# Performance work log

Measured on AMD Instinct MI355X. Metric: run time of the kernel, lower is better.

Reference implementation:

```python
import jax, jax.numpy as jnp
import numpy as np

B, L, D, H, FF = 2, 2048, 1024, 16, 4096


def _xavier(key, out_d, in_d):
    lim = (6.0 / (in_d + out_d)) ** 0.5
    return jax.random.uniform(key, (out_d, in_d), jnp.float32, -lim, lim)


def setup_inputs() -> dict:
    key = jax.random.key(0)
    ks = jax.random.split(key, 7)
    x = jax.random.normal(ks[0], (B, L, D), dtype=jnp.float32)
    wq = _xavier(ks[1], D, D)
    wk = _xavier(ks[2], D, D)
    wv = _xavier(ks[3], D, D)
    wo = _xavier(ks[4], D, D)
    w1 = _xavier(ks[5], FF, D)
    w2 = _xavier(ks[6], D, FF)
    zD = jnp.zeros((D,), jnp.float32)
    return dict(x=x, wq=wq, bq=zD, wk=wk, bk=zD, wv=wv, bv=zD, wo=wo, bo=zD,
                w1=w1, b1=jnp.zeros((FF,), jnp.float32), w2=w2, b2=zD)


def _ln2d(x, eps=1e-5):
    # F.layer_norm(x, x.shape[1:]): normalize jointly over (L, D), no affine
    mu = jnp.mean(x, axis=(1, 2), keepdims=True)
    var = jnp.var(x, axis=(1, 2), keepdims=True)
    return (x - mu) * jax.lax.rsqrt(var + eps)


def reference(x, wq, bq, wk, bk, wv, bv, wo, bo, w1, b1, w2, b2):
    Bx, Lx, Dx = x.shape
    nH = H
    Dh = Dx // nH
    h = _ln2d(x)
    q = (h @ wq.T + bq).reshape(Bx, Lx, nH, Dh).transpose(0, 2, 1, 3)  # (B,H,L,Dh)
    k = (h @ wk.T + bk).reshape(Bx, Lx, nH, Dh).transpose(0, 2, 1, 3)
    v = (h @ wv.T + bv).reshape(Bx, Lx, nH, Dh).transpose(0, 2, 1, 3)
    # NOTE: faithful to source bug: scale = 1/sqrt(key.size(dim=1)) = 1/sqrt(num_heads)
    scale = 1.0 / jnp.sqrt(jnp.asarray(nH, jnp.float32))
    att = jax.nn.softmax(jnp.einsum('bhqd,bhkd->bhqk', q, k) * scale, axis=-1)
    o = jnp.einsum('bhqk,bhkd->bhqd', att, v).transpose(0, 2, 1, 3).reshape(Bx, Lx, Dx)
    o = o @ wo.T + bo
    y = _ln2d(o + x)
    ff = jax.nn.relu(y @ w1.T + b1) @ w2.T + b2
    return ff + x  # second residual adds the ORIGINAL x (as in source)
```

## Files before the change

kernel.cpp:

```cpp
#include <hip/hip_runtime.h>
#include <cstdint>
#include <cstddef>

typedef unsigned short u16;
typedef unsigned int uint;
typedef __bf16 bf16x8 __attribute__((ext_vector_type(8)));
typedef float f32x4 __attribute__((ext_vector_type(4)));

#define BATCH 2
#define SEQ 2048
#define DIM 1024
#define NH 16
#define DH 64
#define FFD 4096
#define MROWS 4096
#define PER_BATCH 2097152

__device__ __forceinline__ u16 f2b(float f) {
  uint u = __builtin_bit_cast(uint, f);
  u += 0x7FFFu + ((u >> 16) & 1u);
  return (u16)(u >> 16);
}

__device__ __forceinline__ uint pkbf2(float a, float b) {
  u16 x = __builtin_bit_cast(u16, (__bf16)a);
  u16 y = __builtin_bit_cast(u16, (__bf16)b);
  return (uint)x | ((uint)y << 16);
}

__device__ __forceinline__ int xcd_swz(int flat, int nwg) {
  return (flat & 7) * (nwg >> 3) + (flat >> 3);
}

#define GLL(gp, lp)                                                            \
  __builtin_amdgcn_global_load_lds(                                            \
      (const __attribute__((address_space(1))) void*)(gp),                     \
      (__attribute__((address_space(3))) void*)(lp), 16, 0, 0)

__global__ __launch_bounds__(256) void cvt4_kernel(const float* __restrict__ s0,
                                                   const float* __restrict__ s1,
                                                   const float* __restrict__ s2,
                                                   const float* __restrict__ s3,
                                                   u16* d0, u16* d1, u16* d2, u16* d3,
                                                   int n) {
  int t = blockIdx.y;
  const float* src = (t == 0) ? s0 : (t == 1) ? s1 : (t == 2) ? s2 : s3;
  u16* dst = (t == 0) ? d0 : (t == 1) ? d1 : (t == 2) ? d2 : d3;
  int i = (blockIdx.x * 256 + threadIdx.x) * 8;
  if (i >= n) return;
  float4 a = *(const float4*)(src + i);
  float4 b = *(const float4*)(src + i + 4);
  uint4 o;
  o.x = f2b(a.x) | ((uint)f2b(a.y) << 16);
  o.y = f2b(a.z) | ((uint)f2b(a.w) << 16);
  o.z = f2b(b.x) | ((uint)f2b(b.y) << 16);
  o.w = f2b(b.z) | ((uint)f2b(b.w) << 16);
  *(uint4*)(dst + i) = o;
}

__global__ __launch_bounds__(256) void reduce_stats_kernel(const float* __restrict__ x,
                                                           float* __restrict__ stats) {
  int b = blockIdx.y;
  const float* p = x + (size_t)b * PER_BATCH;
  float s = 0.f, ss = 0.f;
  int stride = gridDim.x * 256 * 4;
  for (int i = (blockIdx.x * 256 + threadIdx.x) * 4; i < PER_BATCH; i += stride) {
    float4 v = *(const float4*)(p + i);
    s  += (v.x + v.y) + (v.z + v.w);
    ss += (v.x * v.x + v.y * v.y) + (v.z * v.z + v.w * v.w);
  }
#pragma unroll
  for (int m = 32; m; m >>= 1) { s += __shfl_xor(s, m); ss += __shfl_xor(ss, m); }
  __shared__ float red[16];
  int w = threadIdx.x >> 6;
  if ((threadIdx.x & 63) == 0) { red[w] = s; red[8 + w] = ss; }
  __syncthreads();
  if (threadIdx.x == 0) {
    atomicAdd(&stats[b * 2],     red[0] + red[1] + red[2] + red[3]);
    atomicAdd(&stats[b * 2 + 1], red[8] + red[9] + red[10] + red[11]);
  }
}

__global__ __launch_bounds__(256) void ln_apply_kernel(const float* __restrict__ xin,
                                                       const float* __restrict__ stats,
                                                       u16* __restrict__ out) {
  int i = (blockIdx.x * 256 + threadIdx.x) * 4;
  int b = i >> 21;
  const float inv = 1.f / (float)PER_BATCH;
  float mu = stats[b * 2] * inv;
  float var = stats[b * 2 + 1] * inv - mu * mu;
  float rs = rsqrtf(var + 1e-5f);
  float4 v = *(const float4*)(xin + i);
  uint r0 = f2b((v.x - mu) * rs) | ((uint)f2b((v.y - mu) * rs) << 16);
  uint r1 = f2b((v.z - mu) * rs) | ((uint)f2b((v.w - mu) * rs) << 16);
  *(uint2*)(out + i) = make_uint2(r0, r1);
}

template <int TN, int RELU, int RESID, int OUTBF, int DBUF>
__device__ __forceinline__ void gemm_bt_body(const u16* __restrict__ A,
                                             const u16* __restrict__ Bm,
                                             const float* __restrict__ bias,
                                             const float* __restrict__ resid,
                                             void* __restrict__ Cout,
                                             int M, int N, int K,
                                             int m0, int n0, float oscale, int trv) {
  constexpr int AI  = (TN == 128) ? 4 : 2;
  constexpr int BCH = (TN == 128) ? 4 : 2;
  constexpr int NB  = DBUF ? 3 : 1;
  __shared__ __align__(16) u16 As[NB][128 * 64];
  __shared__ __align__(16) u16 Bs[NB][TN * 64];
  const int tid = threadIdx.x;
  const int lane = tid & 63, w = tid >> 6;
  const int wr = (TN == 128) ? (w >> 1) : w;
  const int wc = (TN == 128) ? (w & 1) : 0;
  const int ln = lane & 15, qd = lane >> 4;

  f32x4 acc[AI][4] = {};

  const int lrow = lane >> 3;
  const int scl  = (lane & 7) ^ lrow;
  const u16* Ag = A  + (size_t)(m0 + w * 32 + lrow) * K + scl * 8;
  const u16* Bg = Bm + (size_t)(n0 + w * 8 * BCH + lrow) * K + scl * 8;

  const int co0 = ((qd)     ^ (ln & 7)) * 8;
  const int co1 = ((4 + qd) ^ (ln & 7)) * 8;

  auto STAGE = [&](int buf, int k0) {
#pragma unroll
    for (int r = 0; r < 4; ++r)
      GLL(Ag + (size_t)(r * 8) * K + k0, As[buf] + (w * 4 + r) * 512);
#pragma unroll
    for (int r = 0; r < BCH; ++r)
      GLL(Bg + (size_t)(r * 8) * K + k0, Bs[buf] + (w * BCH + r) * 512);
  };

  auto COMPUTE = [&](int buf) {
#pragma unroll
    for (int kk = 0; kk < 2; ++kk) {
      const int co = kk ? co1 : co0;
      bf16x8 af[AI], bf[4];
#pragma unroll
      for (int t = 0; t < AI; ++t)
        af[t] = *(const bf16x8*)&As[buf][(wr * (AI * 16) + t * 16 + ln) * 64 + co];
#pragma unroll
      for (int t = 0; t < 4; ++t)
        bf[t] = *(const bf16x8*)&Bs[buf][(wc * 64 + t * 16 + ln) * 64 + co];
#pragma unroll
      for (int i = 0; i < AI; ++i)
#pragma unroll
        for (int j = 0; j < 4; ++j)
          acc[i][j] = __builtin_amdgcn_mfma_f32_16x16x32_bf16(af[i], bf[j], acc[i][j], 0, 0, 0);
    }
  };

  if constexpr (NB == 3) {
    const int nk = K >> 6;
    STAGE(0, 0);
    STAGE(1, 64);
    int c = 0, s = 2;
    int t = 0;
    for (; t + 1 < nk; ++t) {
      asm volatile("s_waitcnt vmcnt(6)" ::: "memory");
      __builtin_amdgcn_s_barrier();
      __builtin_amdgcn_sched_barrier(0);
      if (t + 2 < nk) STAGE(s, (t + 2) * 64);
      COMPUTE(c);
      c = (c == 2) ? 0 : c + 1;
      s = (s == 2) ? 0 : s + 1;
    }
    asm volatile("s_waitcnt vmcnt(0)" ::: "memory");
    __builtin_amdgcn_s_barrier();
    __builtin_amdgcn_sched_barrier(0);
    COMPUTE(c);
  } else {
    for (int k0 = 0; k0 < K; k0 += 64) {
      __syncthreads();
      STAGE(0, k0);
      __syncthreads();
      COMPUTE(0);
    }
  }

#pragma unroll
  for (int i = 0; i < AI; ++i) {
    int row = m0 + wr * (AI * 16) + i * 16 + qd * 4;
#pragma unroll
    for (int j = 0; j < 4; ++j) {
      int col = n0 + wc * 64 + j * 16 + ln;
      float bv = bias[col];
      if (trv) {
        union { uint2 u2; u16 us[4]; } pk;
#pragma unroll
        for (int r = 0; r < 4; ++r) pk.us[r] = f2b(acc[i][j][r] + bv);
        *(uint2*)&((u16*)Cout)[(size_t)col * MROWS + row] = pk.u2;
      } else {
#pragma unroll
        for (int r = 0; r < 4; ++r) {
          float v = (acc[i][j][r] + bv) * oscale;
          if (RELU) v = fmaxf(v, 0.f);
          size_t off = (size_t)(row + r) * N + col;
          if (RESID) v += resid[off];
          if (OUTBF) ((u16*)Cout)[off] = f2b(v);
          else       ((float*)Cout)[off] = v;
        }
      }
    }
  }
}

template <int TN, int RELU, int RESID, int OUTBF, int DBUF>
__global__ __launch_bounds__(256) void gemm_bt_kernel(const u16* __restrict__ A,
                                                      const u16* __restrict__ Bm,
                                                      const float* __restrict__ bias,
                                                      const float* __restrict__ resid,
                                                      void* __restrict__ Cout,
                                                      int M, int N, int K) {
  const int nx = gridDim.x;
  const int nwg = nx * gridDim.y;
  const int wid = xcd_swz(blockIdx.x + nx * blockIdx.y, nwg);
  gemm_bt_body<TN, RELU, RESID, OUTBF, DBUF>(A, Bm, bias, resid, Cout,
                                             M, N, K,
                                             (wid / nx) * 128, (wid % nx) * TN,
                                             1.0f, 0);
}

__global__ __launch_bounds__(256) void gemm_qkv_kernel(const u16* __restrict__ A,
                                                       const u16* B0, const u16* B1, const u16* B2,
                                                       const float* c0, const float* c1, const float* c2,
                                                       u16* o0, u16* o1, u16* o2) {
  int z = blockIdx.z;
  const int wid = xcd_swz(blockIdx.x + 16 * blockIdx.y, 512);
  const int m0 = (wid >> 4) * 128, n0 = (wid & 15) * 64;
  const u16* Bm = (z == 0) ? B0 : (z == 1) ? B1 : B2;
  const float* bias = (z == 0) ? c0 : (z == 1) ? c1 : c2;
  u16* Cout = (z == 0) ? o0 : (z == 1) ? o1 : o2;
  const float sc = (z == 0) ? 0.25f : 1.0f;
  gemm_bt_body<64, 0, 0, 1, 1>(A, Bm, bias, nullptr, Cout,
                               MROWS, DIM, DIM, m0, n0, sc, z == 2);
}

template <int RELU>
__global__ __launch_bounds__(512, 2) void gemm256_kernel(const u16* __restrict__ A,
                                                         const u16* __restrict__ Bm,
                                                         const float* __restrict__ bias,
                                                         u16* __restrict__ Cout,
                                                         int M, int N, int K) {
  __shared__ __align__(16) u16 As[2][256 * 64];
  __shared__ __align__(16) u16 Bs[2][256 * 64];
  const int tid = threadIdx.x;
  const int lane = tid & 63, w = tid >> 6;
  const int wr = w >> 2, wc = w & 3;
  const int ln = lane & 15, qd = lane >> 4;

  const int nx = gridDim.x;
  const int nwg = nx * gridDim.y;
  const int wid = xcd_swz(blockIdx.x + nx * blockIdx.y, nwg);
  const int m0 = (wid / nx) * 256, n0 = (wid % nx) * 256;

  f32x4 acc[8][4] = {};

  const int lrow = lane >> 3;
  const int scl  = (lane & 7) ^ lrow;
  const u16* Ag = A  + (size_t)(m0 + w * 32 + lrow) * K + scl * 8;
  const u16* Bg = Bm + (size_t)(n0 + w * 32 + lrow) * K + scl * 8;

  const int co0 = ((qd)     ^ (ln & 7)) * 8;
  const int co1 = ((4 + qd) ^ (ln & 7)) * 8;

  auto STAGE = [&](int buf, int k0) {
#pragma unroll
    for (int r = 0; r < 4; ++r) {
      GLL(Ag + (size_t)(r * 8) * K + k0, As[buf] + (w * 4 + r) * 512);
      GLL(Bg + (size_t)(r * 8) * K + k0, Bs[buf] + (w * 4 + r) * 512);
    }
  };

  auto COMPUTE = [&](int buf) {
#pragma unroll
    for (int kk = 0; kk < 2; ++kk) {
      const int co = kk ? co1 : co0;
      bf16x8 af[8], bf[4];
#pragma unroll
      for (int t = 0; t < 8; ++t)
        af[t] = *(const bf16x8*)&As[buf][(wr * 128 + t * 16 + ln) * 64 + co];
#pragma unroll
      for (int t = 0; t < 4; ++t)
        bf[t] = *(const bf16x8*)&Bs[buf][(wc * 64 + t * 16 + ln) * 64 + co];
      __builtin_amdgcn_s_setprio(1);
#pragma unroll
      for (int i = 0; i < 8; ++i)
#pragma unroll
        for (int j = 0; j < 4; ++j)
          acc[i][j] = __builtin_amdgcn_mfma_f32_16x16x32_bf16(af[i], bf[j], acc[i][j], 0, 0, 0);
      __builtin_amdgcn_s_setprio(0);
    }
  };

  const int nk = K >> 6;
  STAGE(0, 0);
  for (int t = 0; t < nk; ++t) {
    const int p = t & 1;
    __syncthreads();
    if (t + 1 < nk) STAGE(1 - p, (t + 1) * 64);
    COMPUTE(p);
  }

#pragma unroll
  for (int i = 0; i < 8; ++i) {
    int row = m0 + wr * 128 + i * 16 + qd * 4;
#pragma unroll
    for (int j = 0; j < 4; ++j) {
      int col = n0 + wc * 64 + j * 16 + ln;
      float bv = bias[col];
#pragma unroll
      for (int r = 0; r < 4; ++r) {
        float v = acc[i][j][r] + bv;
        if (RELU) v = fmaxf(v, 0.f);
        Cout[(size_t)(row + r) * N + col] = f2b(v);
      }
    }
  }
}

__global__ __launch_bounds__(256, 2) void attn_kernel(const u16* __restrict__ Q,
                                                      const u16* __restrict__ Km,
                                                      const u16* __restrict__ vT,
                                                      u16* __restrict__ O) {
  __shared__ __align__(16) u16 Ks[2][64 * 64];
  __shared__ __align__(16) u16 Vt[2][64 * 64];
  __shared__ __align__(16) u16 Ps[4][32 * 64];

  const int tid = threadIdx.x, lane = tid & 63, w = tid >> 6;
  const int ln = lane & 15, qd = lane >> 4;
  const int flat = blockIdx.x + 16 * (blockIdx.y + 16 * blockIdx.z);
  const int wid = xcd_swz(flat, 512);
  const int qi = wid & 15, head = (wid >> 4) & 15, b = wid >> 8;
  const int wq0 = b * SEQ + qi * 128 + w * 32;
  const int hcol = head * DH;

  bf16x8 qf[2][2];
#pragma unroll
  for (int ti = 0; ti < 2; ++ti)
#pragma unroll
    for (int kk = 0; kk < 2; ++kk)
      qf[ti][kk] = *(const bf16x8*)&Q[(size_t)(wq0 + ti * 16 + ln) * DIM + hcol + kk * 32 + qd * 8];

  union { u16 u[8]; bf16x8 v; } oneu;
#pragma unroll
  for (int e = 0; e < 8; ++e) oneu.u[e] = 0x3F80;
  const bf16x8 vones = oneu.v;

  f32x4 accO[2][4] = {};
  f32x4 accL[2] = {};

  const int srow = lane >> 3;
  const int scl  = (lane & 7) ^ srow;
  const u16* Kg = Km + (size_t)(b * SEQ + w * 16 + srow) * DIM + hcol + scl * 8;
  const u16* Vg = vT + (size_t)(hcol + w * 16 + srow) * MROWS + b * SEQ + scl * 8;
  u16* Pw = Ps[w];
  const int swz = ln & 7;

#pragma unroll
  for (int r = 0; r < 2; ++r) {
    GLL(Kg + (size_t)(r * 8) * DIM,   &Ks[0][(w * 2 + r) * 512]);
    GLL(Vg + (size_t)(r * 8) * MROWS, &Vt[0][(w * 2 + r) * 512]);
  }

  for (int t = 0; t < SEQ / 64; ++t) {
    const int p = t & 1;
    const int kt = t * 64;
    __syncthreads();

    if (t + 1 < SEQ / 64) {
      const int kt2 = kt + 64;
#pragma unroll
      for (int r = 0; r < 2; ++r) {
        GLL(Kg + (size_t)(kt2 + r * 8) * DIM,   &Ks[1 - p][(w * 2 + r) * 512]);
        GLL(Vg + (size_t)(r * 8) * MROWS + kt2, &Vt[1 - p][(w * 2 + r) * 512]);
      }
    }

    f32x4 sacc[4][2] = {};
#pragma unroll
    for (int kk = 0; kk < 2; ++kk) {
      bf16x8 kf[4];
#pragma unroll
      for (int tj = 0; tj < 4; ++tj)
        kf[tj] = *(const bf16x8*)&Ks[p][(tj * 16 + ln) * 64 + (((kk * 4 + qd) ^ swz) * 8)];
      __builtin_amdgcn_s_setprio(1);
#pragma unroll
      for (int tj = 0; tj < 4; ++tj)
#pragma unroll
        for (int ti = 0; ti < 2; ++ti)
          sacc[tj][ti] = __builtin_amdgcn_mfma_f32_16x16x32_bf16(kf[tj], qf[ti][kk], sacc[tj][ti], 0, 0, 0);
      __builtin_amdgcn_s_setprio(0);
    }

#pragma unroll
    for (int tj = 0; tj < 4; ++tj)
#pragma unroll
      for (int ti = 0; ti < 2; ++ti) {
        uint lo = pkbf2(__expf(sacc[tj][ti][0]), __expf(sacc[tj][ti][1]));
        uint hi = pkbf2(__expf(sacc[tj][ti][2]), __expf(sacc[tj][ti][3]));
        *(uint2*)&Pw[(ti * 16 + ln) * 64 + (((2 * tj + (qd >> 1)) ^ swz) * 8) + (qd & 1) * 4] =
            make_uint2(lo, hi);
      }

#pragma unroll
    for (int kk = 0; kk < 2; ++kk) {
      bf16x8 pf[2], vf[4];
#pragma unroll
      for (int ti = 0; ti < 2; ++ti)
        pf[ti] = *(const bf16x8*)&Pw[(ti * 16 + ln) * 64 + (((kk * 4 + qd) ^ swz) * 8)];
#pragma unroll
      for (int tjv = 0; tjv < 4; ++tjv)
        vf[tjv] = *(const bf16x8*)&Vt[p][(tjv * 16 + ln) * 64 + (((kk * 4 + qd) ^ swz) * 8)];
      __builtin_amdgcn_s_setprio(1);
#pragma unroll
      for (int ti = 0; ti < 2; ++ti) {
#pragma unroll
        for (int tjv = 0; tjv < 4; ++tjv)
          accO[ti][tjv] = __builtin_amdgcn_mfma_f32_16x16x32_bf16(pf[ti], vf[tjv], accO[ti][tjv], 0, 0, 0);
        accL[ti] = __builtin_amdgcn_mfma_f32_16x16x32_bf16(pf[ti], vones, accL[ti], 0, 0, 0);
      }
      __builtin_amdgcn_s_setprio(0);
    }
  }

#pragma unroll
  for (int ti = 0; ti < 2; ++ti)
#pragma unroll
    for (int r = 0; r < 4; ++r) {
      float inv = 1.f / accL[ti][r];
#pragma unroll
      for (int tjv = 0; tjv < 4; ++tjv)
        O[(size_t)(wq0 + ti * 16 + qd * 4 + r) * DIM + hcol + tjv * 16 + ln] =
            f2b(accO[ti][tjv][r] * inv);
    }
}

extern "C" void kernel_launch(void* const* d_in, const int* in_sizes, int n_in,
                              void* d_out, int out_size, void* d_ws, size_t ws_size,
                              hipStream_t stream) {
  const float* x  = (const float*)d_in[0];
  const float* wq = (const float*)d_in[1];
  const float* bq = (const float*)d_in[2];
  const float* wk = (const float*)d_in[3];
  const float* bk = (const float*)d_in[4];
  const float* wv = (const float*)d_in[5];
  const float* bv = (const float*)d_in[6];
  const float* wo = (const float*)d_in[7];
  const float* bo = (const float*)d_in[8];
  const float* w1 = (const float*)d_in[9];
  const float* b1 = (const float*)d_in[10];
  const float* w2 = (const float*)d_in[11];
  const float* b2 = (const float*)d_in[12];
  float* out = (float*)d_out;
  char* ws = (char*)d_ws;

  const size_t MB = 1u << 20;
  u16*   h    = (u16*)(ws + 0);
  u16*   q    = (u16*)(ws + 8  * MB);
  u16*   k    = (u16*)(ws + 16 * MB);
  u16*   v    = (u16*)(ws + 24 * MB);
  u16*   o    = (u16*)(ws + 32 * MB);
  u16*   r    = (u16*)(ws + 8  * MB);
  float* ares = (float*)(ws + 40 * MB);
  u16*   wqb  = (u16*)(ws + 56 * MB);
  u16*   wkb  = (u16*)(ws + 58 * MB);
  u16*   wvb  = (u16*)(ws + 60 * MB);
  u16*   wob  = (u16*)(ws + 62 * MB);
  u16*   w1b  = (u16*)(ws + 64 * MB);
  u16*   w2b  = (u16*)(ws + 72 * MB);
  float* stats= (float*)(ws + 80 * MB);
  u16*   y    = h;

  (void)hipMemsetAsync(stats, 0, 64, stream);

  cvt4_kernel<<<dim3(512, 4),  256, 0, stream>>>(wq, wk, wv, wo, wqb, wkb, wvb, wob, DIM * DIM);
  cvt4_kernel<<<dim3(2048, 2), 256, 0, stream>>>(w1, w2, w1, w2, w1b, w2b, w1b, w2b, FFD * DIM);

  reduce_stats_kernel<<<dim3(64, 2), 256, 0, stream>>>(x, stats);
  ln_apply_kernel<<<4096, 256, 0, stream>>>(x, stats, h);

  gemm_qkv_kernel<<<dim3(16, 32, 3), 256, 0, stream>>>(h, wqb, wkb, wvb, bq, bk, bv, q, k, v);

  attn_kernel<<<dim3(16, 16, 2), 256, 0, stream>>>(q, k, v, o);

  gemm_bt_kernel<64, 0, 1, 0, 1><<<dim3(16, 32), 256, 0, stream>>>(o, wob, bo, x, ares, MROWS, DIM, DIM);

  reduce_stats_kernel<<<dim3(64, 2), 256, 0, stream>>>(ares, stats + 4);
  ln_apply_kernel<<<4096, 256, 0, stream>>>(ares, stats + 4, y);

  gemm256_kernel<1><<<dim3(16, 16), 512, 0, stream>>>(y, w1b, b1, r, MROWS, FFD, DIM);

  gemm_bt_kernel<64, 0, 1, 0, 1><<<dim3(16, 32), 256, 0, stream>>>(r, w2b, b2, x, out, MROWS, DIM, FFD);
}
```

Before: 357.1 us.

## Fuse QKV projections into one GEMM sharing A tiles; merge weight conversions

Replaces the z-dimension QKV launch (three separate GEMMs that each reload the same activation tile) with one kernel. Each workgroup loads its 128x64 A tile once and multiplies it against the matching tiles of all three weight matrices, with a double-buffered LDS pipeline. The two weight-conversion launches are also merged into one six-way launch. This cuts redundant A traffic and a launch, at the cost of triple the accumulator registers (96 floats per lane), larger LDS use, lower occupancy, and only 512 workgroups instead of 1536.

```diff
diff --git a/kernel.cpp b/kernel.cpp
--- a/kernel.cpp
+++ b/kernel.cpp
@@ -37,15 +37,20 @@
       (const __attribute__((address_space(1))) void*)(gp),                     \
       (__attribute__((address_space(3))) void*)(lp), 16, 0, 0)
 
-__global__ __launch_bounds__(256) void cvt4_kernel(const float* __restrict__ s0,
+__global__ __launch_bounds__(256) void cvt6_kernel(const float* __restrict__ s0,
                                                    const float* __restrict__ s1,
                                                    const float* __restrict__ s2,
                                                    const float* __restrict__ s3,
-                                                   u16* d0, u16* d1, u16* d2, u16* d3,
-                                                   int n) {
+                                                   const float* __restrict__ s4,
+                                                   const float* __restrict__ s5,
+                                                   u16* d0, u16* d1, u16* d2,
+                                                   u16* d3, u16* d4, u16* d5) {
   int t = blockIdx.y;
-  const float* src = (t == 0) ? s0 : (t == 1) ? s1 : (t == 2) ? s2 : s3;
-  u16* dst = (t == 0) ? d0 : (t == 1) ? d1 : (t == 2) ? d2 : d3;
+  const float* src = (t == 0) ? s0 : (t == 1) ? s1 : (t == 2) ? s2
+                   : (t == 3) ? s3 : (t == 4) ? s4 : s5;
+  u16* dst = (t == 0) ? d0 : (t == 1) ? d1 : (t == 2) ? d2
+           : (t == 3) ? d3 : (t == 4) ? d4 : d5;
+  int n = (t < 4) ? DIM * DIM : FFD * DIM;
   int i = (blockIdx.x * 256 + threadIdx.x) * 8;
   if (i >= n) return;
   float4 a = *(const float4*)(src + i);
@@ -224,19 +229,104 @@
                                              1.0f, 0);
 }
 
-__global__ __launch_bounds__(256) void gemm_qkv_kernel(const u16* __restrict__ A,
-                                                       const u16* B0, const u16* B1, const u16* B2,
-                                                       const float* c0, const float* c1, const float* c2,
-                                                       u16* o0, u16* o1, u16* o2) {
-  int z = blockIdx.z;
+__global__ __launch_bounds__(256) void gemm_qkv3_kernel(const u16* __restrict__ A,
+                                                        const u16* __restrict__ B0,
+                                                        const u16* __restrict__ B1,
+                                                        const u16* __restrict__ B2,
+                                                        const float* __restrict__ c0,
+                                                        const float* __restrict__ c1,
+                                                        const float* __restrict__ c2,
+                                                        u16* o0, u16* o1, u16* o2) {
+  __shared__ __align__(16) u16 As[2][128 * 64];
+  __shared__ __align__(16) u16 Bs[2][3][64 * 64];
+  const int tid = threadIdx.x;
+  const int lane = tid & 63, w = tid >> 6;
+  const int ln = lane & 15, qd = lane >> 4;
+
   const int wid = xcd_swz(blockIdx.x + 16 * blockIdx.y, 512);
   const int m0 = (wid >> 4) * 128, n0 = (wid & 15) * 64;
-  const u16* Bm = (z == 0) ? B0 : (z == 1) ? B1 : B2;
-  const float* bias = (z == 0) ? c0 : (z == 1) ? c1 : c2;
-  u16* Cout = (z == 0) ? o0 : (z == 1) ? o1 : o2;
-  const float sc = (z == 0) ? 0.25f : 1.0f;
-  gemm_bt_body<64, 0, 0, 1, 1>(A, Bm, bias, nullptr, Cout,
-                               MROWS, DIM, DIM, m0, n0, sc, z == 2);
+
+  f32x4 acc[3][2][4] = {};
+
+  const int lrow = lane >> 3;
+  const int scl  = (lane & 7) ^ lrow;
+  const u16* Ag = A + (size_t)(m0 + w * 32 + lrow) * DIM + scl * 8;
+  const u16* Bg[3] = {
+    B0 + (size_t)(n0 + w * 16 + lrow) * DIM + scl * 8,
+    B1 + (size_t)(n0 + w * 16 + lrow) * DIM + scl * 8,
+    B2 + (size_t)(n0 + w * 16 + lrow) * DIM + scl * 8 };
+
+  const int co0 = ((qd)     ^ (ln & 7)) * 8;
+  const int co1 = ((4 + qd) ^ (ln & 7)) * 8;
+
+  auto STAGE = [&](int buf, int k0) {
+#pragma unroll
+    for (int r = 0; r < 4; ++r)
+      GLL(Ag + (size_t)(r * 8) * DIM + k0, As[buf] + (w * 4 + r) * 512);
+#pragma unroll
+    for (int z = 0; z < 3; ++z)
+#pragma unroll
+      for (int r = 0; r < 2; ++r)
+        GLL(Bg[z] + (size_t)(r * 8) * DIM + k0, Bs[buf][z] + (w * 2 + r) * 512);
+  };
+
+  auto COMPUTE = [&](int buf) {
+#pragma unroll
+    for (int kk = 0; kk < 2; ++kk) {
+      const int co = kk ? co1 : co0;
+      bf16x8 af[2];
+#pragma unroll
+      for (int t = 0; t < 2; ++t)
+        af[t] = *(const bf16x8*)&As[buf][(w * 32 + t * 16 + ln) * 64 + co];
+#pragma unroll
+      for (int z = 0; z < 3; ++z) {
+        bf16x8 bf[4];
+#pragma unroll
+        for (int t = 0; t < 4; ++t)
+          bf[t] = *(const bf16x8*)&Bs[buf][z][(t * 16 + ln) * 64 + co];
+#pragma unroll
+        for (int i = 0; i < 2; ++i)
+#pragma unroll
+          for (int j = 0; j < 4; ++j)
+            acc[z][i][j] = __builtin_amdgcn_mfma_f32_16x16x32_bf16(af[i], bf[j], acc[z][i][j], 0, 0, 0);
+      }
+    }
+  };
+
+  const int nk = DIM >> 6;
+  STAGE(0, 0);
+  for (int t = 0; t < nk; ++t) {
+    const int p = t & 1;
+    __syncthreads();
+    if (t + 1 < nk) STAGE(1 - p, (t + 1) * 64);
+    COMPUTE(p);
+  }
+
+#pragma unroll
+  for (int z = 0; z < 3; ++z) {
+    const float* bias = (z == 0) ? c0 : (z == 1) ? c1 : c2;
+    u16* Cout = (z == 0) ? o0 : (z == 1) ? o1 : o2;
+    const float sc = (z == 0) ? 0.25f : 1.0f;
+#pragma unroll
+    for (int i = 0; i < 2; ++i) {
+      int row = m0 + w * 32 + i * 16 + qd * 4;
+#pragma unroll
+      for (int j = 0; j < 4; ++j) {
+        int col = n0 + j * 16 + ln;
+        float bv = bias[col];
+        if (z == 2) {
+          union { uint2 u2; u16 us[4]; } pk;
+#pragma unroll
+          for (int r = 0; r < 4; ++r) pk.us[r] = f2b(acc[z][i][j][r] + bv);
+          *(uint2*)&Cout[(size_t)col * MROWS + row] = pk.u2;
+        } else {
+#pragma unroll
+          for (int r = 0; r < 4; ++r)
+            Cout[(size_t)(row + r) * DIM + col] = f2b((acc[z][i][j][r] + bv) * sc);
+        }
+      }
+    }
+  }
 }
 
 template <int RELU>
@@ -477,13 +567,13 @@
 
   (void)hipMemsetAsync(stats, 0, 64, stream);
 
-  cvt4_kernel<<<dim3(512, 4),  256, 0, stream>>>(wq, wk, wv, wo, wqb, wkb, wvb, wob, DIM * DIM);
-  cvt4_kernel<<<dim3(2048, 2), 256, 0, stream>>>(w1, w2, w1, w2, w1b, w2b, w1b, w2b, FFD * DIM);
+  cvt6_kernel<<<dim3(2048, 6), 256, 0, stream>>>(wq, wk, wv, wo, w1, w2,
+                                                 wqb, wkb, wvb, wob, w1b, w2b);
 
   reduce_stats_kernel<<<dim3(64, 2), 256, 0, stream>>>(x, stats);
   ln_apply_kernel<<<4096, 256, 0, stream>>>(x, stats, h);
 
-  gemm_qkv_kernel<<<dim3(16, 32, 3), 256, 0, stream>>>(h, wqb, wkb, wvb, bq, bk, bv, q, k, v);
+  gemm_qkv3_kernel<<<dim3(16, 32), 256, 0, stream>>>(h, wqb, wkb, wvb, bq, bk, bv, q, k, v);
 
   attn_kernel<<<dim3(16, 16, 2), 256, 0, stream>>>(q, k, v, o);
 
```

New measurement: 351.2 us. No clear change (-1.7%).
